# Kernel tuning notes

Measured on AMD Instinct MI355X. Metric: run time of the kernel, lower is better.

## Reference

```python
import jax, jax.numpy as jnp
import numpy as np
import math

B, L, D, H, F = 4, 2048, 1024, 16, 4096
SF = 5          # sampling_factor
EPS = 1e-12     # LayerNorm eps


def setup_inputs() -> dict:
    key = jax.random.key(0)
    ks = jax.random.split(key, 18)
    s = 0.02
    lin = lambda k, i, o: (jax.random.normal(k, (i, o), jnp.float32) * s)
    log_LK = math.ceil(math.log1p(L))
    U_part = min(SF * L * log_LK, L)  # = L here
    return {
        "x": jax.random.normal(ks[0], (B, L, D), jnp.float32),
        "wq": lin(ks[1], D, D), "bq": jnp.zeros((D,), jnp.float32),
        "wk": lin(ks[2], D, D), "bk": jnp.zeros((D,), jnp.float32),
        "wv": lin(ks[3], D, D), "bv": jnp.zeros((D,), jnp.float32),
        "wo": lin(ks[4], D, D), "bo": jnp.zeros((D,), jnp.float32),
        "w1": lin(ks[5], D, F), "b1": jnp.zeros((F,), jnp.float32),
        "w2": lin(ks[6], F, D), "b2": jnp.zeros((D,), jnp.float32),
        "gamma1": jnp.ones((D,), jnp.float32), "beta1": jnp.zeros((D,), jnp.float32),
        "gamma2": jnp.ones((D,), jnp.float32), "beta2": jnp.zeros((D,), jnp.float32),
        "index_sample": jax.random.randint(ks[7], (U_part,), 0, L, jnp.int32),
    }


def _layernorm(x, g, b):
    m = x.mean(-1, keepdims=True)
    v = ((x - m) ** 2).mean(-1, keepdims=True)  # unbiased=False
    return g * (x - m) / jnp.sqrt(v + EPS) + b


def _prob_sparse_mha(x, wq, bq, wk, bk, wv, bv, wo, bo, index_sample):
    d = D // H
    BH = B * H
    # NOTE: source views q as (B, H, L, d) WITHOUT transpose (quirk kept);
    # k, v are split with the usual (B, L, H, d) -> (B, H, L, d) transpose.
    q = (x @ wq + bq).reshape(BH, L, d)
    k = (x @ wk + bk).reshape(B, L, H, d).transpose(0, 2, 1, 3).reshape(BH, L, d)
    v = (x @ wv + bv).reshape(B, L, H, d).transpose(0, 2, 1, 3).reshape(BH, L, d)

    # --- ProbSparse query selection ---
    K_sample = k[:, index_sample, :]                       # [BH, U_part, d]
    QK = jnp.einsum('bqd,bkd->bqk', q, K_sample)           # [BH, L, U_part]
    M = QK.max(axis=-1) - QK.sum(axis=-1) / L              # sparsity measure
    u = min(SF * math.ceil(math.log1p(L)), L)              # static: 40
    _, M_top = jax.lax.top_k(-M, u)                        # largest=False in src
    Q_reduce = jnp.take_along_axis(q, M_top[:, :, None], axis=1)  # [BH, u, d]

    # --- attention for the selected queries ---
    scores = jnp.einsum('bud,bkd->buk', Q_reduce, k) / math.sqrt(d)
    probs = jax.nn.softmax(scores, axis=-1)
    out_red = jnp.einsum('buk,bkd->bud', probs, v)         # [BH, u, d]

    # scatter reduced outputs back to full length (non-selected rows -> 0)
    full = jnp.zeros_like(q).at[jnp.arange(BH)[:, None], M_top].set(out_red)
    out = full.reshape(B, H, L, d).transpose(0, 2, 1, 3).reshape(B, L, D)
    return out @ wo + bo


def reference(x, wq, bq, wk, bk, wv, bv, wo, bo, w1, b1, w2, b2,
              gamma1, beta1, gamma2, beta2, index_sample):
    a = _prob_sparse_mha(x, wq, bq, wk, bk, wv, bv, wo, bo, index_sample)
    x1 = _layernorm(x + a, gamma1, beta1)          # dropout = identity (eval)
    f = jnp.maximum(x1 @ w1 + b1, 0.0) @ w2 + b2   # FFN (ReLU)
    return _layernorm(x1 + f, gamma2, beta2)
```

## Files before the change

kernel.cpp:

```cpp
#include <hip/hip_runtime.h>
#include <float.h>
#include <math.h>

#define L_SEQ 2048
#define D_MODEL 1024
#define N_HEAD 16
#define HD 64
#define N_BH 64
#define U_TOP 40

using bf16x8 = __attribute__((ext_vector_type(8))) short;
using f32x4  = __attribute__((ext_vector_type(4))) float;

__device__ __forceinline__ unsigned short f2bf(float f) {
    unsigned int u = __builtin_bit_cast(unsigned int, f);
    u += 0x7fff + ((u >> 16) & 1);
    return (unsigned short)(u >> 16);
}
__device__ __forceinline__ float bf2f(unsigned short h) {
    unsigned int u = ((unsigned int)h) << 16;
    return __builtin_bit_cast(float, u);
}

__device__ __forceinline__ void gload_lds16(const void* g, void* l) {
    __builtin_amdgcn_global_load_lds(
        (const __attribute__((address_space(1))) unsigned int*)g,
        (__attribute__((address_space(3))) unsigned int*)l, 16, 0, 0);
}

__device__ __forceinline__ void xcd_tiles(int& bx, int& by) {
    const int nwgx = gridDim.x;
    const int nwg = nwgx * gridDim.y;
    int bid = blockIdx.y * nwgx + blockIdx.x;
    int lb = (bid & 7) * (nwg >> 3) + (bid >> 3);
    bx = lb % nwgx;
    by = lb / nwgx;
}

template<bool OUTBF16, bool RELU, bool ACCUM>
__global__ void __launch_bounds__(256)
gemm_bf16(const unsigned short* __restrict__ A, int lda,
          const unsigned short* __restrict__ BT, int ldbt,
          void* __restrict__ Cp, int ldc, int K,
          const float* __restrict__ bias)
{
    __shared__ short As[4096];
    __shared__ short Bs[4096];
    const int tid = threadIdx.x;
    const int w = tid >> 6, l = tid & 63;
    int bx, by;
    xcd_tiles(bx, by);
    const int wm = w >> 1, wn = w & 1;

    f32x4 acc[4][4] = {};

    const unsigned short* a_src[2];
    const unsigned short* b_src[2];
#pragma unroll
    for (int g = 0; g < 2; ++g) {
        int r = w * 32 + g * 16 + (l >> 2);
        int kc = (l & 3) ^ ((r >> 1) & 3);
        a_src[g] = A + (size_t)(by * 128 + r) * lda + kc * 8;
        b_src[g] = BT + (size_t)(bx * 128 + r) * ldbt + kc * 8;
    }
    short* As_w = As + w * 1024;
    short* Bs_w = Bs + w * 1024;

    const int lr = l & 15, lg = l >> 4;

    for (int k0 = 0; k0 < K; k0 += 32) {
        __syncthreads();
        gload_lds16(a_src[0] + k0, As_w);
        gload_lds16(a_src[1] + k0, As_w + 512);
        gload_lds16(b_src[0] + k0, Bs_w);
        gload_lds16(b_src[1] + k0, Bs_w + 512);
        __syncthreads();

        bf16x8 af[4], bg[4];
#pragma unroll
        for (int m = 0; m < 4; ++m) {
            int row = wm * 64 + m * 16 + lr;
            int off = row * 64 + ((lg ^ ((row >> 1) & 3)) << 4);
            af[m] = *(const bf16x8*)((const char*)As + off);
        }
#pragma unroll
        for (int n = 0; n < 4; ++n) {
            int row = wn * 64 + n * 16 + lr;
            int off = row * 64 + ((lg ^ ((row >> 1) & 3)) << 4);
            bg[n] = *(const bf16x8*)((const char*)Bs + off);
        }
#pragma unroll
        for (int m = 0; m < 4; ++m)
#pragma unroll
            for (int n = 0; n < 4; ++n)
                acc[m][n] = __builtin_amdgcn_mfma_f32_16x16x32_bf16(
                    af[m], bg[n], acc[m][n], 0, 0, 0);
    }

    float bcol[4];
#pragma unroll
    for (int n = 0; n < 4; ++n) {
        int colg = bx * 128 + wn * 64 + n * 16 + lr;
        bcol[n] = bias ? bias[colg] : 0.f;
    }
#pragma unroll
    for (int m = 0; m < 4; ++m) {
#pragma unroll
        for (int n = 0; n < 4; ++n) {
            int colg = bx * 128 + wn * 64 + n * 16 + lr;
#pragma unroll
            for (int r = 0; r < 4; ++r) {
                int rowg = by * 128 + wm * 64 + m * 16 + lg * 4 + r;
                float v = acc[m][n][r] + bcol[n];
                if (RELU) v = fmaxf(v, 0.f);
                if (OUTBF16) {
                    ((unsigned short*)Cp)[(size_t)rowg * ldc + colg] = f2bf(v);
                } else {
                    float* C = (float*)Cp;
                    if (ACCUM) v += C[(size_t)rowg * ldc + colg];
                    C[(size_t)rowg * ldc + colg] = v;
                }
            }
        }
    }
}

__global__ void __launch_bounds__(256)
gemm_bf16_split(const unsigned short* __restrict__ Ah,
                const unsigned short* __restrict__ Al, int lda,
                const unsigned short* __restrict__ BhT,
                const unsigned short* __restrict__ BlT, int ldbt,
                unsigned short* __restrict__ CP, int K,
                const float* __restrict__ bias)
{
    __shared__ short Ash[4096], Asl[4096], Bsh[4096], Bsl[4096];
    const int tid = threadIdx.x;
    const int w = tid >> 6, l = tid & 63;
    int bx, by;
    xcd_tiles(bx, by);
    const int wm = w >> 1, wn = w & 1;

    f32x4 acc[4][4] = {};

    size_t a_off[2], b_off[2];
#pragma unroll
    for (int g = 0; g < 2; ++g) {
        int r = w * 32 + g * 16 + (l >> 2);
        int kc = (l & 3) ^ ((r >> 1) & 3);
        a_off[g] = (size_t)(by * 128 + r) * lda + kc * 8;
        b_off[g] = (size_t)(bx * 128 + r) * ldbt + kc * 8;
    }
    const int wb = w * 1024;
    const int lr = l & 15, lg = l >> 4;

    for (int k0 = 0; k0 < K; k0 += 32) {
        __syncthreads();
#pragma unroll
        for (int g = 0; g < 2; ++g) {
            gload_lds16(Ah + a_off[g] + k0, Ash + wb + g * 512);
            gload_lds16(Al + a_off[g] + k0, Asl + wb + g * 512);
            gload_lds16(BhT + b_off[g] + k0, Bsh + wb + g * 512);
            gload_lds16(BlT + b_off[g] + k0, Bsl + wb + g * 512);
        }
        __syncthreads();

        bf16x8 afh[4], afl[4], bgh[4], bgl[4];
#pragma unroll
        for (int m = 0; m < 4; ++m) {
            int row = wm * 64 + m * 16 + lr;
            int off = row * 64 + ((lg ^ ((row >> 1) & 3)) << 4);
            afh[m] = *(const bf16x8*)((const char*)Ash + off);
            afl[m] = *(const bf16x8*)((const char*)Asl + off);
        }
#pragma unroll
        for (int n = 0; n < 4; ++n) {
            int row = wn * 64 + n * 16 + lr;
            int off = row * 64 + ((lg ^ ((row >> 1) & 3)) << 4);
            bgh[n] = *(const bf16x8*)((const char*)Bsh + off);
            bgl[n] = *(const bf16x8*)((const char*)Bsl + off);
        }
#pragma unroll
        for (int m = 0; m < 4; ++m)
#pragma unroll
            for (int n = 0; n < 4; ++n) {
                acc[m][n] = __builtin_amdgcn_mfma_f32_16x16x32_bf16(
                    afh[m], bgh[n], acc[m][n], 0, 0, 0);
                acc[m][n] = __builtin_amdgcn_mfma_f32_16x16x32_bf16(
                    afh[m], bgl[n], acc[m][n], 0, 0, 0);
                acc[m][n] = __builtin_amdgcn_mfma_f32_16x16x32_bf16(
                    afl[m], bgh[n], acc[m][n], 0, 0, 0);
            }
    }

    float bcol[4];
#pragma unroll
    for (int n = 0; n < 4; ++n)
        bcol[n] = bias[bx * 128 + wn * 64 + n * 16 + lr];
    const int cg = bx * 2 + wn;
#pragma unroll
    for (int m = 0; m < 4; ++m)
#pragma unroll
        for (int n = 0; n < 4; ++n) {
            int cwi = n * 16 + lr;
#pragma unroll
            for (int r = 0; r < 4; ++r) {
                int rowg = by * 128 + wm * 64 + m * 16 + lg * 4 + r;
                float v = acc[m][n][r] + bcol[n];
                unsigned short hh = f2bf(v);
                unsigned short ll = f2bf(v - bf2f(hh));
                size_t ad = (size_t)rowg * 2048 + cg * 128 + cwi;
                CP[ad] = hh;
                CP[ad + 64] = ll;
            }
        }
}

__global__ void __launch_bounds__(256)
preprocess(const float* __restrict__ x,
           const float* __restrict__ wq, const float* __restrict__ wk,
           const float* __restrict__ wv, const float* __restrict__ wo,
           unsigned short* __restrict__ xh, unsigned short* __restrict__ xl,
           unsigned short* __restrict__ wqhT, unsigned short* __restrict__ wqlT,
           unsigned short* __restrict__ wkhT, unsigned short* __restrict__ wklT,
           unsigned short* __restrict__ wvT, unsigned short* __restrict__ woT)
{
    __shared__ float t[32][33];
    const int bid = blockIdx.x, tid = threadIdx.x;
    if (bid < 8192) {
        size_t i = (size_t)bid * 1024 + tid * 4;
        float4 v = *(const float4*)(x + i);
        ushort4 h, l2;
        h.x = f2bf(v.x); l2.x = f2bf(v.x - bf2f(h.x));
        h.y = f2bf(v.y); l2.y = f2bf(v.y - bf2f(h.y));
        h.z = f2bf(v.z); l2.z = f2bf(v.z - bf2f(h.z));
        h.w = f2bf(v.w); l2.w = f2bf(v.w - bf2f(h.w));
        *(ushort4*)(xh + i) = h;
        *(ushort4*)(xl + i) = l2;
        return;
    }
    const int grp = (bid - 8192) >> 10;
    const int b2 = (bid - 8192) & 1023;
    const int bx = (b2 & 31) * 32, by = (b2 >> 5) * 32;
    const float* in = (grp == 0) ? wq : (grp == 1) ? wk : (grp == 2) ? wv : wo;
    const int lx = tid & 31, ly = tid >> 5;
#pragma unroll
    for (int r = 0; r < 4; ++r)
        t[ly + r * 8][lx] = in[(size_t)(by + ly + r * 8) * 1024 + bx + lx];
    __syncthreads();
#pragma unroll
    for (int r = 0; r < 4; ++r) {
        int oc = ly + r * 8;
        float f = t[lx][oc];
        size_t od = (size_t)(bx + oc) * 1024 + by + lx;
        unsigned short hh = f2bf(f);
        if (grp == 0) { wqhT[od] = hh; wqlT[od] = f2bf(f - bf2f(hh)); }
        else if (grp == 1) { wkhT[od] = hh; wklT[od] = f2bf(f - bf2f(hh)); }
        else if (grp == 2) wvT[od] = hh;
        else woT[od] = hh;
    }
}

__global__ void __launch_bounds__(256)
tconv(const float* __restrict__ in, int R, int C, unsigned short* __restrict__ out)
{
    __shared__ float t[32][33];
    const int bx = blockIdx.x * 32;
    const int by = blockIdx.y * 32;
    const int lx = threadIdx.x & 31, ly = threadIdx.x >> 5;
#pragma unroll
    for (int r = 0; r < 4; ++r)
        t[ly + r * 8][lx] = in[(size_t)(by + ly + r * 8) * C + bx + lx];
    __syncthreads();
#pragma unroll
    for (int r = 0; r < 4; ++r) {
        int oc = ly + r * 8;
        out[(size_t)(bx + oc) * R + by + lx] = f2bf(t[lx][oc]);
    }
}

__global__ void __launch_bounds__(256)
gather_ks(const unsigned short* __restrict__ KP, const int* __restrict__ idxs,
          unsigned short* __restrict__ KS)
{
    const int bh = blockIdx.x, b = bh >> 4, h = bh & 15;
    const int r0 = blockIdx.y * 256;
    const int s = threadIdx.x & 15, jr = threadIdx.x >> 4;
#pragma unroll
    for (int p = 0; p < 16; ++p) {
        int j = r0 + p * 16 + jr;
        int idx = idxs[j];
        int kc = (s & 7) ^ (j & 7);
        const unsigned short* src = KP + (size_t)(b * 2048 + idx) * 2048
                                  + h * 128 + ((s & 8) << 3) + kc * 8;
        *(bf16x8*)(KS + ((size_t)bh * 2048 + j) * 128 + s * 8) =
            *(const bf16x8*)src;
    }
}

__global__ void __launch_bounds__(256)
mstat_mfma2(const unsigned short* __restrict__ QP,
            const unsigned short* __restrict__ KS,
            float* __restrict__ Mout)
{
    __shared__ char lds[32768];
    const int tid = threadIdx.x, w = tid >> 6, l = tid & 63;
    const int bh = blockIdx.x, qt = blockIdx.y;
    const int i0 = qt * 128;
    const int lr = l & 15, lg = l >> 4;

    bf16x8 af[2][2][2];
#pragma unroll
    for (int half = 0; half < 2; ++half) {
        __syncthreads();
#pragma unroll
        for (int it = 0; it < 4; ++it) {
            int rq = w * 32 + it * 8 + (l >> 3);
            int i = i0 + rq;
            int kc = (l & 7) ^ (rq & 7);
            gload_lds16(QP + (size_t)(bh * 128 + (i >> 4)) * 2048
                           + (i & 15) * 128 + half * 64 + kc * 8,
                        lds + w * 4096 + it * 1024);
        }
        __syncthreads();
#pragma unroll
        for (int m = 0; m < 2; ++m) {
            int rq = w * 32 + m * 16 + lr;
#pragma unroll
            for (int ks = 0; ks < 2; ++ks) {
                int c = (ks * 4 + lg) ^ (rq & 7);
                af[m][ks][half] = *(const bf16x8*)(lds + rq * 128 + (c << 4));
            }
        }
    }
    __syncthreads();

    float mx[2][4], sm[2][4];
#pragma unroll
    for (int m = 0; m < 2; ++m)
#pragma unroll
        for (int r = 0; r < 4; ++r) { mx[m][r] = -FLT_MAX; sm[m][r] = 0.f; }

    const unsigned short* ksbase = KS + (size_t)bh * (2048 * 128);

#pragma unroll
    for (int it = 0; it < 4; ++it)
        gload_lds16(ksbase + w * 2048 + it * 512 + l * 8,
                    lds + w * 4096 + it * 1024);

    for (int jt = 0; jt < 32; ++jt) {
        const int cur = jt & 1;
        __syncthreads();
        if (jt + 1 < 32) {
#pragma unroll
            for (int it = 0; it < 4; ++it)
                gload_lds16(ksbase + (size_t)(jt + 1) * 8192 + w * 2048 + it * 512 + l * 8,
                            lds + (cur ^ 1) * 16384 + w * 4096 + it * 1024);
        }
        const char* kb = lds + cur * 16384;
#pragma unroll
        for (int n = 0; n < 4; ++n) {
            int jr = n * 16 + lr;
            bf16x8 bgh[2], bgl[2];
#pragma unroll
            for (int ks = 0; ks < 2; ++ks) {
                int c = (ks * 4 + lg) ^ (jr & 7);
                bgh[ks] = *(const bf16x8*)(kb + jr * 256 + (c << 4));
                bgl[ks] = *(const bf16x8*)(kb + jr * 256 + (c << 4) + 128);
            }
#pragma unroll
            for (int m = 0; m < 2; ++m) {
                f32x4 a = {};
                a = __builtin_amdgcn_mfma_f32_16x16x32_bf16(af[m][0][0], bgh[0], a, 0, 0, 0);
                a = __builtin_amdgcn_mfma_f32_16x16x32_bf16(af[m][0][1], bgh[0], a, 0, 0, 0);
                a = __builtin_amdgcn_mfma_f32_16x16x32_bf16(af[m][0][0], bgl[0], a, 0, 0, 0);
                a = __builtin_amdgcn_mfma_f32_16x16x32_bf16(af[m][1][0], bgh[1], a, 0, 0, 0);
                a = __builtin_amdgcn_mfma_f32_16x16x32_bf16(af[m][1][1], bgh[1], a, 0, 0, 0);
                a = __builtin_amdgcn_mfma_f32_16x16x32_bf16(af[m][1][0], bgl[1], a, 0, 0, 0);
#pragma unroll
                for (int r = 0; r < 4; ++r) {
                    mx[m][r] = fmaxf(mx[m][r], a[r]);
                    sm[m][r] += a[r];
                }
            }
        }
    }

#pragma unroll
    for (int m = 0; m < 2; ++m)
#pragma unroll
        for (int r = 0; r < 4; ++r) {
            float a = mx[m][r], s = sm[m][r];
#pragma unroll
            for (int mask = 1; mask < 16; mask <<= 1) {
                a = fmaxf(a, __shfl_xor(a, mask));
                s += __shfl_xor(s, mask);
            }
            if (lr == 0) {
                int row = i0 + w * 32 + m * 16 + lg * 4 + r;
                Mout[(size_t)bh * L_SEQ + row] = a - s * (1.0f / 2048.0f);
            }
        }
}

__global__ void __launch_bounds__(256)
topk_kernel(const float* __restrict__ M, int* __restrict__ Mtop)
{
    __shared__ float mv[L_SEQ];
    __shared__ float wv_[4];
    __shared__ int wi_[4];
    const int bh = blockIdx.x;
    const int tid = threadIdx.x;
    for (int j = tid; j < L_SEQ; j += 256) mv[j] = M[(size_t)bh * L_SEQ + j];
    __syncthreads();
    for (int u = 0; u < U_TOP; ++u) {
        float best = FLT_MAX;
        int bi = 1 << 30;
        for (int j = tid; j < L_SEQ; j += 256) {
            float v = mv[j];
            if (v < best || (v == best && j < bi)) { best = v; bi = j; }
        }
#pragma unroll
        for (int off = 32; off; off >>= 1) {
            float ov = __shfl_down(best, off);
            int oi = __shfl_down(bi, off);
            if (ov < best || (ov == best && oi < bi)) { best = ov; bi = oi; }
        }
        if ((tid & 63) == 0) { wv_[tid >> 6] = best; wi_[tid >> 6] = bi; }
        __syncthreads();
        if (tid == 0) {
            for (int w = 1; w < 4; ++w)
                if (wv_[w] < best || (wv_[w] == best && wi_[w] < bi)) { best = wv_[w]; bi = wi_[w]; }
            Mtop[bh * U_TOP + u] = bi;
            mv[bi] = FLT_MAX;
        }
        __syncthreads();
    }
}

__global__ void __launch_bounds__(256)
attn_fused(const unsigned short* __restrict__ QP,
           const unsigned short* __restrict__ KP,
           const unsigned short* __restrict__ V,
           const int* __restrict__ Mtop,
           unsigned short* __restrict__ PART,
           float* __restrict__ ML)
{
    __shared__ unsigned short Qs[64 * 64];
    __shared__ unsigned short Ks[128 * 64];
    __shared__ unsigned short Vt[64 * 128];
    __shared__ unsigned short Pb[64 * 128];
    const int sp = blockIdx.x, bh = blockIdx.y;
    const int b = bh >> 4, h = bh & 15;
    const int tid = threadIdx.x, w = tid >> 6, l = tid & 63;
    const int lr = l & 15, lg = l >> 4;

#pragma unroll
    for (int is = 0; is < 2; ++is) {
        int row = w * 16 + is * 8 + (l >> 3);
        int u = row < U_TOP ? row : U_TOP - 1;
        int lsel = Mtop[bh * U_TOP + u];
        int cg = (l & 7) ^ (row & 7);
        gload_lds16(QP + (size_t)(bh * 128 + (lsel >> 4)) * 2048
                       + (lsel & 15) * 128 + cg * 8,
                    &Qs[(w * 16 + is * 8) * 64]);
    }
    __syncthreads();

    bf16x8 af[2];
    {
        int row = w * 16 + lr;
#pragma unroll
        for (int ks = 0; ks < 2; ++ks) {
            int c = (ks * 4 + lg) ^ (row & 7);
            af[ks] = *(const bf16x8*)((const char*)Qs + row * 128 + (c << 4));
        }
    }

    float m_run[4], l_run[4];
    f32x4 oacc[4] = {};
#pragma unroll
    for (int r = 0; r < 4; ++r) { m_run[r] = -FLT_MAX; l_run[r] = 0.f; }

    for (int t = sp * 4; t < sp * 4 + 4; ++t) {
        const int j0 = t * 128;
        __syncthreads();

#pragma unroll
        for (int is = 0; is < 4; ++is) {
            int kr = w * 32 + is * 8 + (l >> 3);
            int cg = (l & 7) ^ (kr & 7);
            gload_lds16(KP + (size_t)(b * 2048 + j0 + kr) * 2048 + h * 128 + cg * 8,
                        &Ks[(w * 32 + is * 8) * 64]);
        }
        {
            int key = tid & 127, dh = (tid >> 7) * 32;
            const unsigned short* vsrc =
                V + (((size_t)(b * L_SEQ + j0 + key)) << 10) + (h << 6) + dh;
            bf16x8 vv[4];
#pragma unroll
            for (int i = 0; i < 4; ++i) vv[i] = *(const bf16x8*)(vsrc + i * 8);
            int ck = key >> 3, klo = (key & 7) * 2;
#pragma unroll
            for (int i = 0; i < 4; ++i)
#pragma unroll
                for (int j = 0; j < 8; ++j) {
                    int d = dh + i * 8 + j;
                    *(unsigned short*)((char*)Vt + d * 256 +
                                       ((ck ^ (d & 7)) << 4) + klo) =
                        (unsigned short)vv[i][j];
                }
        }
        __syncthreads();

        f32x4 sc[8] = {};
#pragma unroll
        for (int ks = 0; ks < 2; ++ks)
#pragma unroll
            for (int n = 0; n < 8; ++n) {
                int krow = n * 16 + lr;
                int c = (ks * 4 + lg) ^ (krow & 7);
                bf16x8 bf = *(const bf16x8*)((const char*)Ks + krow * 128 + (c << 4));
                sc[n] = __builtin_amdgcn_mfma_f32_16x16x32_bf16(af[ks], bf, sc[n], 0, 0, 0);
            }

        float rs[4];
#pragma unroll
        for (int r = 0; r < 4; ++r) {
            int row = w * 16 + lg * 4 + r;
            float mt = -FLT_MAX;
#pragma unroll
            for (int n = 0; n < 8; ++n) mt = fmaxf(mt, sc[n][r]);
            mt *= 0.125f;
#pragma unroll
            for (int mask = 1; mask < 16; mask <<= 1)
                mt = fmaxf(mt, __shfl_xor(mt, mask));
            float mn = fmaxf(m_run[r], mt);
            rs[r] = expf(m_run[r] - mn);
            float ls = 0.f;
            int rsw = row & 7;
#pragma unroll
            for (int n = 0; n < 8; ++n) {
                float p = expf(sc[n][r] * 0.125f - mn);
                ls += p;
                int ckp = (lr >> 3) + 2 * n;
                *(unsigned short*)((char*)Pb + row * 256 +
                                   ((ckp ^ rsw) << 4) + (lr & 7) * 2) = f2bf(p);
            }
#pragma unroll
            for (int mask = 1; mask < 16; mask <<= 1) ls += __shfl_xor(ls, mask);
            l_run[r] = l_run[r] * rs[r] + ls;
            m_run[r] = mn;
        }
        __syncthreads();

#pragma unroll
        for (int n = 0; n < 4; ++n)
#pragma unroll
            for (int r = 0; r < 4; ++r) oacc[n][r] *= rs[r];
#pragma unroll
        for (int ks = 0; ks < 4; ++ks) {
            int arow = w * 16 + lr;
            int ca = (lg + ks * 4) ^ (arow & 7);
            bf16x8 pa = *(const bf16x8*)((const char*)Pb + arow * 256 + (ca << 4));
#pragma unroll
            for (int n = 0; n < 4; ++n) {
                int d = n * 16 + lr;
                int cb = (lg + ks * 4) ^ (d & 7);
                bf16x8 vb = *(const bf16x8*)((const char*)Vt + d * 256 + (cb << 4));
                oacc[n] = __builtin_amdgcn_mfma_f32_16x16x32_bf16(pa, vb, oacc[n], 0, 0, 0);
            }
        }
    }

    const int pbase = (bh * 4 + sp) * 64;
#pragma unroll
    for (int r = 0; r < 4; ++r) {
        int row = w * 16 + lg * 4 + r;
#pragma unroll
        for (int n = 0; n < 4; ++n)
            PART[(size_t)(pbase + row) * 64 + n * 16 + lr] = f2bf(oacc[n][r]);
        if (lr == 0) {
            ML[(size_t)(pbase + row) * 2 + 0] = m_run[r];
            ML[(size_t)(pbase + row) * 2 + 1] = l_run[r];
        }
    }
}

__global__ void __launch_bounds__(256)
woscatter(const unsigned short* __restrict__ PART,
          const float* __restrict__ ML,
          const unsigned short* __restrict__ woT,
          const int* __restrict__ Mtop,
          float* __restrict__ Ab)
{
    const int bh = blockIdx.x, b = bh >> 4, h = bh & 15;
    const int tid = threadIdx.x, w = tid >> 6, l = tid & 63;
    const int lr = l & 15, lg = l >> 4;

    bf16x8 af[3][2];
#pragma unroll
    for (int m = 0; m < 3; ++m) {
        int row = m * 16 + lr;
        float ms[4], ls[4];
#pragma unroll
        for (int s = 0; s < 4; ++s) {
            ms[s] = ML[(size_t)((bh * 4 + s) * 64 + row) * 2 + 0];
            ls[s] = ML[(size_t)((bh * 4 + s) * 64 + row) * 2 + 1];
        }
        float M = fmaxf(fmaxf(ms[0], ms[1]), fmaxf(ms[2], ms[3]));
        float wgt[4], L = 0.f;
#pragma unroll
        for (int s = 0; s < 4; ++s) { wgt[s] = expf(ms[s] - M); L += wgt[s] * ls[s]; }
        float invL = 1.f / L;
#pragma unroll
        for (int ks = 0; ks < 2; ++ks) {
            float a8[8] = {};
#pragma unroll
            for (int s = 0; s < 4; ++s) {
                bf16x8 po = *(const bf16x8*)(PART +
                    (size_t)((bh * 4 + s) * 64 + row) * 64 + (ks * 4 + lg) * 8);
#pragma unroll
                for (int j = 0; j < 8; ++j)
                    a8[j] += wgt[s] * bf2f((unsigned short)po[j]);
            }
            bf16x8 fr;
#pragma unroll
            for (int j = 0; j < 8; ++j) fr[j] = (short)f2bf(a8[j] * invL);
            af[m][ks] = fr;
        }
    }

    int lsel[3][4];
#pragma unroll
    for (int m = 0; m < 3; ++m)
#pragma unroll
        for (int r = 0; r < 4; ++r) {
            int row = m * 16 + lg * 4 + r;
            lsel[m][r] = row < U_TOP ? Mtop[bh * U_TOP + row] : -1;
        }

    for (int nn = 0; nn < 16; ++nn) {
        int ng = w * 16 + nn;
        bf16x8 bg[2];
#pragma unroll
        for (int ks = 0; ks < 2; ++ks)
            bg[ks] = *(const bf16x8*)(woT + (size_t)(ng * 16 + lr) * 1024
                                      + h * 64 + (ks * 4 + lg) * 8);
        f32x4 a[3] = {};
#pragma unroll
        for (int m = 0; m < 3; ++m)
#pragma unroll
            for (int ks = 0; ks < 2; ++ks)
                a[m] = __builtin_amdgcn_mfma_f32_16x16x32_bf16(af[m][ks], bg[ks], a[m], 0, 0, 0);
#pragma unroll
        for (int m = 0; m < 3; ++m)
#pragma unroll
            for (int r = 0; r < 4; ++r)
                if (lsel[m][r] >= 0)
                    atomicAdd(Ab + (size_t)(b * 2048 + lsel[m][r]) * 1024
                              + ng * 16 + lr, a[m][r]);
    }
}

template<bool WB16, bool BADD>
__global__ void __launch_bounds__(256)
ln_kernel(const float* __restrict__ X, const float* __restrict__ A,
          const float* __restrict__ badd,
          const float* __restrict__ g, const float* __restrict__ be,
          float* __restrict__ out, unsigned short* __restrict__ out16)
{
    __shared__ float wred[4];
    const int row = blockIdx.x, tid = threadIdx.x;
    float4 xv = *(const float4*)(X + (size_t)row * D_MODEL + tid * 4);
    float4 av = *(const float4*)(A + (size_t)row * D_MODEL + tid * 4);
    float v0 = xv.x + av.x, v1 = xv.y + av.y, v2 = xv.z + av.z, v3 = xv.w + av.w;
    if (BADD) {
        float4 bb = *(const float4*)(badd + tid * 4);
        v0 += bb.x; v1 += bb.y; v2 += bb.z; v3 += bb.w;
    }

    float s = v0 + v1 + v2 + v3;
#pragma unroll
    for (int off = 32; off; off >>= 1) s += __shfl_down(s, off);
    if ((tid & 63) == 0) wred[tid >> 6] = s;
    __syncthreads();
    float mean = (wred[0] + wred[1] + wred[2] + wred[3]) * (1.f / 1024.f);
    __syncthreads();

    float d0 = v0 - mean, d1 = v1 - mean, d2 = v2 - mean, d3 = v3 - mean;
    float q = d0 * d0 + d1 * d1 + d2 * d2 + d3 * d3;
#pragma unroll
    for (int off = 32; off; off >>= 1) q += __shfl_down(q, off);
    if ((tid & 63) == 0) wred[tid >> 6] = q;
    __syncthreads();
    float var = (wred[0] + wred[1] + wred[2] + wred[3]) * (1.f / 1024.f);
    float rstd = rsqrtf(var + 1e-12f);

    float4 gv = *(const float4*)(g + tid * 4);
    float4 bv = *(const float4*)(be + tid * 4);
    float4 o;
    o.x = gv.x * d0 * rstd + bv.x;
    o.y = gv.y * d1 * rstd + bv.y;
    o.z = gv.z * d2 * rstd + bv.z;
    o.w = gv.w * d3 * rstd + bv.w;
    *(float4*)(out + (size_t)row * D_MODEL + tid * 4) = o;
    if (WB16) {
        ushort4 ob;
        ob.x = f2bf(o.x); ob.y = f2bf(o.y); ob.z = f2bf(o.z); ob.w = f2bf(o.w);
        *(ushort4*)(out16 + (size_t)row * D_MODEL + tid * 4) = ob;
    }
}

extern "C" void kernel_launch(void* const* d_in, const int* in_sizes, int n_in,
                              void* d_out, int out_size, void* d_ws, size_t ws_size,
                              hipStream_t stream)
{
    const float* x   = (const float*)d_in[0];
    const float* wq  = (const float*)d_in[1];
    const float* bq  = (const float*)d_in[2];
    const float* wk  = (const float*)d_in[3];
    const float* bk  = (const float*)d_in[4];
    const float* wv  = (const float*)d_in[5];
    const float* bv  = (const float*)d_in[6];
    const float* wo  = (const float*)d_in[7];
    const float* bo  = (const float*)d_in[8];
    const float* w1  = (const float*)d_in[9];
    const float* b1  = (const float*)d_in[10];
    const float* w2  = (const float*)d_in[11];
    const float* b2  = (const float*)d_in[12];
    const float* g1  = (const float*)d_in[13];
    const float* be1 = (const float*)d_in[14];
    const float* g2  = (const float*)d_in[15];
    const float* be2 = (const float*)d_in[16];
    const int*  idxs = (const int*)d_in[17];

    char* ws  = (char*)d_ws;
    char* dob = (char*)d_out;
    const size_t MB = 1u << 20;

    unsigned short* QP   = (unsigned short*)(ws);
    unsigned short* KP   = (unsigned short*)(ws + 32 * MB);
    unsigned short* xh   = (unsigned short*)(ws + 64 * MB);
    unsigned short* xl   = (unsigned short*)(ws + 80 * MB);
    unsigned short* KS   = (unsigned short*)(ws + 64 * MB);
    float*          Ab   = (float*)(ws + 64 * MB);
    float*          x1f  = (float*)(ws + 96 * MB);
    unsigned short* x1b  = (unsigned short*)(ws);
    unsigned short* w1T  = (unsigned short*)(ws + 16 * MB);
    unsigned short* w2T  = (unsigned short*)(ws + 24 * MB);
    unsigned short* HID  = (unsigned short*)(ws + 32 * MB);

    unsigned short* woT  = (unsigned short*)(dob);
    unsigned short* wqhT = (unsigned short*)(dob + 2 * MB);
    unsigned short* wqlT = (unsigned short*)(dob + 4 * MB);
    unsigned short* wkhT = (unsigned short*)(dob + 6 * MB);
    unsigned short* wklT = (unsigned short*)(dob + 8 * MB);
    unsigned short* wvT  = (unsigned short*)(dob + 10 * MB);
    float*          Mb   = (float*)(dob + 12 * MB);
    int*            Mtop = (int*)(dob + 12 * MB + 768 * 1024);
    unsigned short* Vb   = (unsigned short*)(dob + 13 * MB);
    unsigned short* PART = (unsigned short*)(dob + 29 * MB);
    float*          ML   = (float*)(dob + 31 * MB);
    float*          F    = (float*)d_out;

    dim3 blk(256);
    dim3 g_gemm(8, 64);

    preprocess<<<dim3(12288), blk, 0, stream>>>(x, wq, wk, wv, wo,
                                                xh, xl, wqhT, wqlT, wkhT, wklT,
                                                wvT, woT);

    gemm_bf16_split<<<g_gemm, blk, 0, stream>>>(xh, xl, 1024, wqhT, wqlT, 1024,
                                                QP, 1024, bq);
    gemm_bf16_split<<<g_gemm, blk, 0, stream>>>(xh, xl, 1024, wkhT, wklT, 1024,
                                                KP, 1024, bk);
    gemm_bf16<true, false, false><<<g_gemm, blk, 0, stream>>>(xh, 1024, wvT, 1024,
                                                              Vb, 1024, 1024, bv);

    gather_ks<<<dim3(64, 8), blk, 0, stream>>>(KP, idxs, KS);
    mstat_mfma2<<<dim3(64, 16), blk, 0, stream>>>(QP, KS, Mb);
    topk_kernel<<<dim3(64), blk, 0, stream>>>(Mb, Mtop);

    hipMemsetAsync(Ab, 0, 32 * MB, stream);
    attn_fused<<<dim3(4, N_BH), blk, 0, stream>>>(QP, KP, Vb, Mtop, PART, ML);
    woscatter<<<dim3(N_BH), blk, 0, stream>>>(PART, ML, woT, Mtop, Ab);

    ln_kernel<true, true><<<dim3(8192), blk, 0, stream>>>(x, Ab, bo, g1, be1, x1f, x1b);

    tconv<<<dim3(128, 32), blk, 0, stream>>>(w1, 1024, 4096, w1T);
    tconv<<<dim3(32, 128), blk, 0, stream>>>(w2, 4096, 1024, w2T);

    gemm_bf16<true, true, false><<<dim3(32, 64), blk, 0, stream>>>(
        x1b, 1024, w1T, 1024, HID, 4096, 1024, b1);
    gemm_bf16<false, false, false><<<g_gemm, blk, 0, stream>>>(
        HID, 4096, w2T, 4096, F, 1024, 4096, b2);

    ln_kernel<false, false><<<dim3(8192), blk, 0, stream>>>(x1f, F, nullptr, g2, be2,
                                                            (float*)d_out, nullptr);
}
```

Baseline: 737.8 us.

## Merge QKV GEMMs into one launch, split-K the FFN down-projection, slim LayerNorm

Q, K and V projections now run in one kernel over a 24x64 grid, with blocks picking their weights by group instead of three separate launches. The second FFN GEMM splits K into two halves across blockIdx.z, writing two fp32 partials that the final LayerNorm sums. This fills more CUs than the 512-block grid did. The first LayerNorm now writes only bf16 output, and the second reads that bf16 residual instead of an fp32 copy. This cuts memory traffic but rounds the residual to bf16, which may lower accuracy.

```diff
diff --git a/kernel.cpp b/kernel.cpp
--- a/kernel.cpp
+++ b/kernel.cpp
@@ -37,12 +37,12 @@
     by = lb / nwgx;
 }
 
-template<bool OUTBF16, bool RELU, bool ACCUM>
+template<bool OUTBF16, bool RELU, bool KSPLIT>
 __global__ void __launch_bounds__(256)
 gemm_bf16(const unsigned short* __restrict__ A, int lda,
           const unsigned short* __restrict__ BT, int ldbt,
           void* __restrict__ Cp, int ldc, int K,
-          const float* __restrict__ bias)
+          const float* __restrict__ bias, void* __restrict__ Cp2)
 {
     __shared__ short As[4096];
     __shared__ short Bs[4096];
@@ -50,6 +50,8 @@
     const int w = tid >> 6, l = tid & 63;
     int bx, by;
     xcd_tiles(bx, by);
+    const int kz = KSPLIT ? blockIdx.z : 0;
+    const size_t koff = (size_t)kz * K;
     const int wm = w >> 1, wn = w & 1;
 
     f32x4 acc[4][4] = {};
@@ -60,8 +62,8 @@
     for (int g = 0; g < 2; ++g) {
         int r = w * 32 + g * 16 + (l >> 2);
         int kc = (l & 3) ^ ((r >> 1) & 3);
-        a_src[g] = A + (size_t)(by * 128 + r) * lda + kc * 8;
-        b_src[g] = BT + (size_t)(bx * 128 + r) * ldbt + kc * 8;
+        a_src[g] = A + (size_t)(by * 128 + r) * lda + koff + kc * 8;
+        b_src[g] = BT + (size_t)(bx * 128 + r) * ldbt + koff + kc * 8;
     }
     short* As_w = As + w * 1024;
     short* Bs_w = Bs + w * 1024;
@@ -97,11 +99,13 @@
                     af[m], bg[n], acc[m][n], 0, 0, 0);
     }
 
+    const float* bias_eff = (KSPLIT && kz) ? nullptr : bias;
+    void* Cp_eff = (KSPLIT && kz) ? Cp2 : Cp;
     float bcol[4];
 #pragma unroll
     for (int n = 0; n < 4; ++n) {
         int colg = bx * 128 + wn * 64 + n * 16 + lr;
-        bcol[n] = bias ? bias[colg] : 0.f;
+        bcol[n] = bias_eff ? bias_eff[colg] : 0.f;
     }
 #pragma unroll
     for (int m = 0; m < 4; ++m) {
@@ -114,11 +118,9 @@
                 float v = acc[m][n][r] + bcol[n];
                 if (RELU) v = fmaxf(v, 0.f);
                 if (OUTBF16) {
-                    ((unsigned short*)Cp)[(size_t)rowg * ldc + colg] = f2bf(v);
+                    ((unsigned short*)Cp_eff)[(size_t)rowg * ldc + colg] = f2bf(v);
                 } else {
-                    float* C = (float*)Cp;
-                    if (ACCUM) v += C[(size_t)rowg * ldc + colg];
-                    C[(size_t)rowg * ldc + colg] = v;
+                    ((float*)Cp_eff)[(size_t)rowg * ldc + colg] = v;
                 }
             }
         }
@@ -126,93 +128,149 @@
 }
 
 __global__ void __launch_bounds__(256)
-gemm_bf16_split(const unsigned short* __restrict__ Ah,
-                const unsigned short* __restrict__ Al, int lda,
-                const unsigned short* __restrict__ BhT,
-                const unsigned short* __restrict__ BlT, int ldbt,
-                unsigned short* __restrict__ CP, int K,
-                const float* __restrict__ bias)
+gemm_qkv(const unsigned short* __restrict__ xh, const unsigned short* __restrict__ xl,
+         const unsigned short* __restrict__ wqhT, const unsigned short* __restrict__ wqlT,
+         const unsigned short* __restrict__ wkhT, const unsigned short* __restrict__ wklT,
+         const unsigned short* __restrict__ wvT,
+         unsigned short* __restrict__ QP, unsigned short* __restrict__ KP,
+         unsigned short* __restrict__ Vb,
+         const float* __restrict__ bq, const float* __restrict__ bk,
+         const float* __restrict__ bv)
 {
     __shared__ short Ash[4096], Asl[4096], Bsh[4096], Bsl[4096];
     const int tid = threadIdx.x;
     const int w = tid >> 6, l = tid & 63;
-    int bx, by;
-    xcd_tiles(bx, by);
+    int bxf, by;
+    xcd_tiles(bxf, by);
+    const int grp = bxf >> 3;
+    const int bx = bxf & 7;
     const int wm = w >> 1, wn = w & 1;
-
-    f32x4 acc[4][4] = {};
+    const int wb = w * 1024;
+    const int lr = l & 15, lg = l >> 4;
 
     size_t a_off[2], b_off[2];
 #pragma unroll
     for (int g = 0; g < 2; ++g) {
         int r = w * 32 + g * 16 + (l >> 2);
         int kc = (l & 3) ^ ((r >> 1) & 3);
-        a_off[g] = (size_t)(by * 128 + r) * lda + kc * 8;
-        b_off[g] = (size_t)(bx * 128 + r) * ldbt + kc * 8;
-    }
-    const int wb = w * 1024;
-    const int lr = l & 15, lg = l >> 4;
-
-    for (int k0 = 0; k0 < K; k0 += 32) {
-        __syncthreads();
-#pragma unroll
-        for (int g = 0; g < 2; ++g) {
-            gload_lds16(Ah + a_off[g] + k0, Ash + wb + g * 512);
-            gload_lds16(Al + a_off[g] + k0, Asl + wb + g * 512);
-            gload_lds16(BhT + b_off[g] + k0, Bsh + wb + g * 512);
-            gload_lds16(BlT + b_off[g] + k0, Bsl + wb + g * 512);
-        }
-        __syncthreads();
-
-        bf16x8 afh[4], afl[4], bgh[4], bgl[4];
-#pragma unroll
-        for (int m = 0; m < 4; ++m) {
-            int row = wm * 64 + m * 16 + lr;
-            int off = row * 64 + ((lg ^ ((row >> 1) & 3)) << 4);
-            afh[m] = *(const bf16x8*)((const char*)Ash + off);
-            afl[m] = *(const bf16x8*)((const char*)Asl + off);
-        }
-#pragma unroll
-        for (int n = 0; n < 4; ++n) {
-            int row = wn * 64 + n * 16 + lr;
-            int off = row * 64 + ((lg ^ ((row >> 1) & 3)) << 4);
-            bgh[n] = *(const bf16x8*)((const char*)Bsh + off);
-            bgl[n] = *(const bf16x8*)((const char*)Bsl + off);
-        }
+        a_off[g] = (size_t)(by * 128 + r) * 1024 + kc * 8;
+        b_off[g] = (size_t)(bx * 128 + r) * 1024 + kc * 8;
+    }
+
+    f32x4 acc[4][4] = {};
+
+    if (grp < 2) {
+        const unsigned short* BhT = grp ? wkhT : wqhT;
+        const unsigned short* BlT = grp ? wklT : wqlT;
+        for (int k0 = 0; k0 < 1024; k0 += 32) {
+            __syncthreads();
+#pragma unroll
+            for (int g = 0; g < 2; ++g) {
+                gload_lds16(xh + a_off[g] + k0, Ash + wb + g * 512);
+                gload_lds16(xl + a_off[g] + k0, Asl + wb + g * 512);
+                gload_lds16(BhT + b_off[g] + k0, Bsh + wb + g * 512);
+                gload_lds16(BlT + b_off[g] + k0, Bsl + wb + g * 512);
+            }
+            __syncthreads();
+
+            bf16x8 afh[4], afl[4], bgh[4], bgl[4];
+#pragma unroll
+            for (int m = 0; m < 4; ++m) {
+                int row = wm * 64 + m * 16 + lr;
+                int off = row * 64 + ((lg ^ ((row >> 1) & 3)) << 4);
+                afh[m] = *(const bf16x8*)((const char*)Ash + off);
+                afl[m] = *(const bf16x8*)((const char*)Asl + off);
+            }
+#pragma unroll
+            for (int n = 0; n < 4; ++n) {
+                int row = wn * 64 + n * 16 + lr;
+                int off = row * 64 + ((lg ^ ((row >> 1) & 3)) << 4);
+                bgh[n] = *(const bf16x8*)((const char*)Bsh + off);
+                bgl[n] = *(const bf16x8*)((const char*)Bsl + off);
+            }
+#pragma unroll
+            for (int m = 0; m < 4; ++m)
+#pragma unroll
+                for (int n = 0; n < 4; ++n) {
+                    acc[m][n] = __builtin_amdgcn_mfma_f32_16x16x32_bf16(
+                        afh[m], bgh[n], acc[m][n], 0, 0, 0);
+                    acc[m][n] = __builtin_amdgcn_mfma_f32_16x16x32_bf16(
+                        afh[m], bgl[n], acc[m][n], 0, 0, 0);
+                    acc[m][n] = __builtin_amdgcn_mfma_f32_16x16x32_bf16(
+                        afl[m], bgh[n], acc[m][n], 0, 0, 0);
+                }
+        }
+
+        const float* bias = grp ? bk : bq;
+        unsigned short* CP = grp ? KP : QP;
+        float bcol[4];
+#pragma unroll
+        for (int n = 0; n < 4; ++n)
+            bcol[n] = bias[bx * 128 + wn * 64 + n * 16 + lr];
+        const int cg = bx * 2 + wn;
 #pragma unroll
         for (int m = 0; m < 4; ++m)
 #pragma unroll
             for (int n = 0; n < 4; ++n) {
-                acc[m][n] = __builtin_amdgcn_mfma_f32_16x16x32_bf16(
-                    afh[m], bgh[n], acc[m][n], 0, 0, 0);
-                acc[m][n] = __builtin_amdgcn_mfma_f32_16x16x32_bf16(
-                    afh[m], bgl[n], acc[m][n], 0, 0, 0);
-                acc[m][n] = __builtin_amdgcn_mfma_f32_16x16x32_bf16(
-                    afl[m], bgh[n], acc[m][n], 0, 0, 0);
-            }
-    }
-
-    float bcol[4];
-#pragma unroll
-    for (int n = 0; n < 4; ++n)
-        bcol[n] = bias[bx * 128 + wn * 64 + n * 16 + lr];
-    const int cg = bx * 2 + wn;
-#pragma unroll
-    for (int m = 0; m < 4; ++m)
-#pragma unroll
-        for (int n = 0; n < 4; ++n) {
-            int cwi = n * 16 + lr;
-#pragma unroll
-            for (int r = 0; r < 4; ++r) {
-                int rowg = by * 128 + wm * 64 + m * 16 + lg * 4 + r;
-                float v = acc[m][n][r] + bcol[n];
-                unsigned short hh = f2bf(v);
-                unsigned short ll = f2bf(v - bf2f(hh));
-                size_t ad = (size_t)rowg * 2048 + cg * 128 + cwi;
-                CP[ad] = hh;
-                CP[ad + 64] = ll;
-            }
-        }
+                int cwi = n * 16 + lr;
+#pragma unroll
+                for (int r = 0; r < 4; ++r) {
+                    int rowg = by * 128 + wm * 64 + m * 16 + lg * 4 + r;
+                    float v = acc[m][n][r] + bcol[n];
+                    unsigned short hh = f2bf(v);
+                    unsigned short ll = f2bf(v - bf2f(hh));
+                    size_t ad = (size_t)rowg * 2048 + cg * 128 + cwi;
+                    CP[ad] = hh;
+                    CP[ad + 64] = ll;
+                }
+            }
+    } else {
+        for (int k0 = 0; k0 < 1024; k0 += 32) {
+            __syncthreads();
+#pragma unroll
+            for (int g = 0; g < 2; ++g) {
+                gload_lds16(xh + a_off[g] + k0, Ash + wb + g * 512);
+                gload_lds16(wvT + b_off[g] + k0, Bsh + wb + g * 512);
+            }
+            __syncthreads();
+
+            bf16x8 af[4], bg[4];
+#pragma unroll
+            for (int m = 0; m < 4; ++m) {
+                int row = wm * 64 + m * 16 + lr;
+                int off = row * 64 + ((lg ^ ((row >> 1) & 3)) << 4);
+                af[m] = *(const bf16x8*)((const char*)Ash + off);
+            }
+#pragma unroll
+            for (int n = 0; n < 4; ++n) {
+                int row = wn * 64 + n * 16 + lr;
+                int off = row * 64 + ((lg ^ ((row >> 1) & 3)) << 4);
+                bg[n] = *(const bf16x8*)((const char*)Bsh + off);
+            }
+#pragma unroll
+            for (int m = 0; m < 4; ++m)
+#pragma unroll
+                for (int n = 0; n < 4; ++n)
+                    acc[m][n] = __builtin_amdgcn_mfma_f32_16x16x32_bf16(
+                        af[m], bg[n], acc[m][n], 0, 0, 0);
+        }
+
+        float bcol[4];
+#pragma unroll
+        for (int n = 0; n < 4; ++n)
+            bcol[n] = bv[bx * 128 + wn * 64 + n * 16 + lr];
+#pragma unroll
+        for (int m = 0; m < 4; ++m)
+#pragma unroll
+            for (int n = 0; n < 4; ++n) {
+                int colg = bx * 128 + wn * 64 + n * 16 + lr;
+#pragma unroll
+                for (int r = 0; r < 4; ++r) {
+                    int rowg = by * 128 + wm * 64 + m * 16 + lg * 4 + r;
+                    Vb[(size_t)rowg * 1024 + colg] = f2bf(acc[m][n][r] + bcol[n]);
+                }
+            }
+    }
 }
 
 __global__ void __launch_bounds__(256)
@@ -662,22 +720,60 @@
     }
 }
 
-template<bool WB16, bool BADD>
-__global__ void __launch_bounds__(256)
-ln_kernel(const float* __restrict__ X, const float* __restrict__ A,
-          const float* __restrict__ badd,
-          const float* __restrict__ g, const float* __restrict__ be,
-          float* __restrict__ out, unsigned short* __restrict__ out16)
+__global__ void __launch_bounds__(256)
+ln1_kernel(const float* __restrict__ X, const float* __restrict__ A,
+           const float* __restrict__ badd,
+           const float* __restrict__ g, const float* __restrict__ be,
+           unsigned short* __restrict__ out16)
 {
     __shared__ float wred[4];
     const int row = blockIdx.x, tid = threadIdx.x;
     float4 xv = *(const float4*)(X + (size_t)row * D_MODEL + tid * 4);
     float4 av = *(const float4*)(A + (size_t)row * D_MODEL + tid * 4);
-    float v0 = xv.x + av.x, v1 = xv.y + av.y, v2 = xv.z + av.z, v3 = xv.w + av.w;
-    if (BADD) {
-        float4 bb = *(const float4*)(badd + tid * 4);
-        v0 += bb.x; v1 += bb.y; v2 += bb.z; v3 += bb.w;
-    }
+    float4 bb = *(const float4*)(badd + tid * 4);
+    float v0 = xv.x + av.x + bb.x, v1 = xv.y + av.y + bb.y;
+    float v2 = xv.z + av.z + bb.z, v3 = xv.w + av.w + bb.w;
+
+    float s = v0 + v1 + v2 + v3;
+#pragma unroll
+    for (int off = 32; off; off >>= 1) s += __shfl_down(s, off);
+    if ((tid & 63) == 0) wred[tid >> 6] = s;
+    __syncthreads();
+    float mean = (wred[0] + wred[1] + wred[2] + wred[3]) * (1.f / 1024.f);
+    __syncthreads();
+
+    float d0 = v0 - mean, d1 = v1 - mean, d2 = v2 - mean, d3 = v3 - mean;
+    float q = d0 * d0 + d1 * d1 + d2 * d2 + d3 * d3;
+#pragma unroll
+    for (int off = 32; off; off >>= 1) q += __shfl_down(q, off);
+    if ((tid & 63) == 0) wred[tid >> 6] = q;
+    __syncthreads();
+    float var = (wred[0] + wred[1] + wred[2] + wred[3]) * (1.f / 1024.f);
+    float rstd = rsqrtf(var + 1e-12f);
+
+    float4 gv = *(const float4*)(g + tid * 4);
+    float4 bv = *(const float4*)(be + tid * 4);
+    ushort4 ob;
+    ob.x = f2bf(gv.x * d0 * rstd + bv.x);
+    ob.y = f2bf(gv.y * d1 * rstd + bv.y);
+    ob.z = f2bf(gv.z * d2 * rstd + bv.z);
+    ob.w = f2bf(gv.w * d3 * rstd + bv.w);
+    *(ushort4*)(out16 + (size_t)row * D_MODEL + tid * 4) = ob;
+}
+
+__global__ void __launch_bounds__(256)
+ln2_kernel(const unsigned short* __restrict__ X16, const float* __restrict__ F0,
+           const float* __restrict__ F1,
+           const float* __restrict__ g, const float* __restrict__ be,
+           float* __restrict__ out)
+{
+    __shared__ float wred[4];
+    const int row = blockIdx.x, tid = threadIdx.x;
+    ushort4 xv = *(const ushort4*)(X16 + (size_t)row * D_MODEL + tid * 4);
+    float4 a0 = *(const float4*)(F0 + (size_t)row * D_MODEL + tid * 4);
+    float4 a1 = *(const float4*)(F1 + (size_t)row * D_MODEL + tid * 4);
+    float v0 = bf2f(xv.x) + a0.x + a1.x, v1 = bf2f(xv.y) + a0.y + a1.y;
+    float v2 = bf2f(xv.z) + a0.z + a1.z, v3 = bf2f(xv.w) + a0.w + a1.w;
 
     float s = v0 + v1 + v2 + v3;
 #pragma unroll
@@ -704,11 +800,6 @@
     o.z = gv.z * d2 * rstd + bv.z;
     o.w = gv.w * d3 * rstd + bv.w;
     *(float4*)(out + (size_t)row * D_MODEL + tid * 4) = o;
-    if (WB16) {
-        ushort4 ob;
-        ob.x = f2bf(o.x); ob.y = f2bf(o.y); ob.z = f2bf(o.z); ob.w = f2bf(o.w);
-        *(ushort4*)(out16 + (size_t)row * D_MODEL + tid * 4) = ob;
-    }
 }
 
 extern "C" void kernel_launch(void* const* d_in, const int* in_sizes, int n_in,
@@ -744,11 +835,11 @@
     unsigned short* xl   = (unsigned short*)(ws + 80 * MB);
     unsigned short* KS   = (unsigned short*)(ws + 64 * MB);
     float*          Ab   = (float*)(ws + 64 * MB);
-    float*          x1f  = (float*)(ws + 96 * MB);
     unsigned short* x1b  = (unsigned short*)(ws);
     unsigned short* w1T  = (unsigned short*)(ws + 16 * MB);
     unsigned short* w2T  = (unsigned short*)(ws + 24 * MB);
     unsigned short* HID  = (unsigned short*)(ws + 32 * MB);
+    float*          F1   = (float*)(ws + 96 * MB);
 
     unsigned short* woT  = (unsigned short*)(dob);
     unsigned short* wqhT = (unsigned short*)(dob + 2 * MB);
@@ -761,21 +852,16 @@
     unsigned short* Vb   = (unsigned short*)(dob + 13 * MB);
     unsigned short* PART = (unsigned short*)(dob + 29 * MB);
     float*          ML   = (float*)(dob + 31 * MB);
-    float*          F    = (float*)d_out;
+    float*          F0   = (float*)d_out;
 
     dim3 blk(256);
-    dim3 g_gemm(8, 64);
 
     preprocess<<<dim3(12288), blk, 0, stream>>>(x, wq, wk, wv, wo,
                                                 xh, xl, wqhT, wqlT, wkhT, wklT,
                                                 wvT, woT);
 
-    gemm_bf16_split<<<g_gemm, blk, 0, stream>>>(xh, xl, 1024, wqhT, wqlT, 1024,
-                                                QP, 1024, bq);
-    gemm_bf16_split<<<g_gemm, blk, 0, stream>>>(xh, xl, 1024, wkhT, wklT, 1024,
-                                                KP, 1024, bk);
-    gemm_bf16<true, false, false><<<g_gemm, blk, 0, stream>>>(xh, 1024, wvT, 1024,
-                                                              Vb, 1024, 1024, bv);
+    gemm_qkv<<<dim3(24, 64), blk, 0, stream>>>(xh, xl, wqhT, wqlT, wkhT, wklT,
+                                               wvT, QP, KP, Vb, bq, bk, bv);
 
     gather_ks<<<dim3(64, 8), blk, 0, stream>>>(KP, idxs, KS);
     mstat_mfma2<<<dim3(64, 16), blk, 0, stream>>>(QP, KS, Mb);
@@ -785,16 +871,15 @@
     attn_fused<<<dim3(4, N_BH), blk, 0, stream>>>(QP, KP, Vb, Mtop, PART, ML);
     woscatter<<<dim3(N_BH), blk, 0, stream>>>(PART, ML, woT, Mtop, Ab);
 
-    ln_kernel<true, true><<<dim3(8192), blk, 0, stream>>>(x, Ab, bo, g1, be1, x1f, x1b);
+    ln1_kernel<<<dim3(8192), blk, 0, stream>>>(x, Ab, bo, g1, be1, x1b);
 
     tconv<<<dim3(128, 32), blk, 0, stream>>>(w1, 1024, 4096, w1T);
     tconv<<<dim3(32, 128), blk, 0, stream>>>(w2, 4096, 1024, w2T);
 
     gemm_bf16<true, true, false><<<dim3(32, 64), blk, 0, stream>>>(
-        x1b, 1024, w1T, 1024, HID, 4096, 1024, b1);
-    gemm_bf16<false, false, false><<<g_gemm, blk, 0, stream>>>(
-        HID, 4096, w2T, 4096, F, 1024, 4096, b2);
-
-    ln_kernel<false, false><<<dim3(8192), blk, 0, stream>>>(x1f, F, nullptr, g2, be2,
-                                                            (float*)d_out, nullptr);
-}
+        x1b, 1024, w1T, 1024, HID, 4096, 1024, b1, nullptr);
+    gemm_bf16<false, false, true><<<dim3(8, 64, 2), blk, 0, stream>>>(
+        HID, 4096, w2T, 4096, F0, 1024, 2048, b2, F1);
+
+    ln2_kernel<<<dim3(8192), blk, 0, stream>>>(x1b, F0, F1, g2, be2, (float*)d_out);
+}
```

After: 731.3 us. Within noise of the previous version (-0.9%).
